# Performance work log

Measured on AMD Instinct MI355X. Metric: run time of the kernel, lower is better.

Reference implementation:

```python
import jax, jax.numpy as jnp
import numpy as np

DIM_MODEL = 1024
NUM_HEADS = 16
DROPOUT_P = 0.5
SCALE = float(np.sqrt(DIM_MODEL // NUM_HEADS))  # NOTE: source MULTIPLIES by this (unusual but faithful)
DROP_KEY = jax.random.key(42)


def setup_inputs() -> dict:
    key = jax.random.key(0)
    ks = jax.random.split(key, 9)
    B, LQ, LK, D = 4, 2048, 2048, DIM_MODEL
    s = 1.0 / np.sqrt(D)
    return {
        "query": jax.random.normal(ks[0], (B, LQ, D), jnp.float32),
        "key": jax.random.normal(ks[1], (B, LK, D), jnp.float32),
        "value": jax.random.normal(ks[2], (B, LK, D), jnp.float32),
        "Wq": jax.random.normal(ks[3], (D, D), jnp.float32) * s,
        "bq": jax.random.normal(ks[4], (D,), jnp.float32) * s,
        "Wk": jax.random.normal(ks[5], (D, D), jnp.float32) * s,
        "bk": jax.random.normal(ks[6], (D,), jnp.float32) * s,
        "Wv": jax.random.normal(ks[7], (D, D), jnp.float32) * s,
        "bv": jax.random.normal(ks[8], (D,), jnp.float32) * s,
    }


def reference(query, key, value, Wq, bq, Wk, bk, Wv, bv):
    # Linear projections (W stored as [in, out])
    q = jnp.einsum('bqd,de->bqe', query, Wq) + bq
    k = jnp.einsum('bkd,de->bke', key, Wk) + bk
    v = jnp.einsum('bkd,de->bke', value, Wv) + bv
    # scores scaled by MULTIPLYING sqrt(d_head), per source
    scores = jnp.einsum('bqe,bke->bqk', q, k) * SCALE
    probs = jax.nn.softmax(scores, axis=-1)
    # dropout (train mode, p=0.5), deterministic fixed key for reproducibility
    keep = jax.random.bernoulli(DROP_KEY, 1.0 - DROPOUT_P, probs.shape)
    probs = jnp.where(keep, probs / (1.0 - DROPOUT_P), 0.0)
    return jnp.einsum('bqk,bke->bqe', probs, v)
```

## Files before the change

### kernel.cpp

```cpp
#include <hip/hip_runtime.h>
#include <math.h>

#define BATCH  4
#define LSEQ   2048
#define DMODEL 1024
#define MROWS  (BATCH * LSEQ)
#define SCORE_SCALE 8.0f

#define THREEFRY_PARTITIONABLE 1

typedef __bf16 bf16_t;
typedef bf16_t bf16x8 __attribute__((ext_vector_type(8)));
typedef bf16_t bf16x4 __attribute__((ext_vector_type(4)));
typedef float  f32x4  __attribute__((ext_vector_type(4)));

#define LDSP(p) ((__attribute__((address_space(3))) void*)(p))
#define GLBP(p) ((const __attribute__((address_space(1))) void*)(p))

__device__ __forceinline__ unsigned rotl32(unsigned x, int r) {
    return (x << r) | (x >> (32 - r));
}

__device__ __forceinline__ void threefry2x32(unsigned k0, unsigned k1,
                                             unsigned x0, unsigned x1,
                                             unsigned& o0, unsigned& o1) {
    const unsigned ks0 = k0, ks1 = k1, ks2 = k0 ^ k1 ^ 0x1BD11BDAu;
    x0 += ks0; x1 += ks1;
#define TF_R(r) { x0 += x1; x1 = rotl32(x1, r); x1 ^= x0; }
    TF_R(13) TF_R(15) TF_R(26) TF_R(6)
    x0 += ks1; x1 += ks2 + 1u;
    TF_R(17) TF_R(29) TF_R(16) TF_R(24)
    x0 += ks2; x1 += ks0 + 2u;
    TF_R(13) TF_R(15) TF_R(26) TF_R(6)
    x0 += ks0; x1 += ks1 + 3u;
    TF_R(17) TF_R(29) TF_R(16) TF_R(24)
    x0 += ks1; x1 += ks2 + 4u;
    TF_R(13) TF_R(15) TF_R(26) TF_R(6)
    x0 += ks2; x1 += ks0 + 5u;
#undef TF_R
    o0 = x0; o1 = x1;
}

__device__ __forceinline__ bool dropout_keep(unsigned n) {
    unsigned o0, o1;
#if THREEFRY_PARTITIONABLE
    threefry2x32(0u, 42u, 0u, n, o0, o1);
    unsigned bits = o0 ^ o1;
#else
    const unsigned HALF = (unsigned)(BATCH * LSEQ) * (unsigned)LSEQ / 2u;
    unsigned c0 = (n < HALF) ? n : (n - HALF);
    unsigned c1 = (n < HALF) ? (n + HALF) : n;
    threefry2x32(0u, 42u, c0, c1, o0, o1);
    unsigned bits = (n < HALF) ? o0 : o1;
#endif
    return bits < 0x80000000u;
}

__global__ __launch_bounds__(256)
void split_f32(const float* __restrict__ X0, const float* __restrict__ X1,
               bf16_t* __restrict__ hi, bf16_t* __restrict__ lo, int n) {
    const int y = blockIdx.y;
    const float* X = y ? X1 : X0;
    long long i = (long long)(blockIdx.x * 256 + threadIdx.x) * 4;
    if (i >= n) return;
    float4 v = *(const float4*)(X + i);
    bf16x4 h, l;
    h[0] = (bf16_t)v.x; l[0] = (bf16_t)(v.x - (float)h[0]);
    h[1] = (bf16_t)v.y; l[1] = (bf16_t)(v.y - (float)h[1]);
    h[2] = (bf16_t)v.z; l[2] = (bf16_t)(v.z - (float)h[2]);
    h[3] = (bf16_t)v.w; l[3] = (bf16_t)(v.w - (float)h[3]);
    *(bf16x4*)(hi + (long long)y * n + i) = h;
    *(bf16x4*)(lo + (long long)y * n + i) = l;
}

__global__ __launch_bounds__(256)
void cvt_bf16(const float* __restrict__ X, bf16_t* __restrict__ Y, int n) {
    long long i = (long long)(blockIdx.x * 256 + threadIdx.x) * 8;
    if (i >= n) return;
    float4 a = *(const float4*)(X + i);
    float4 b = *(const float4*)(X + i + 4);
    bf16x8 o;
    o[0] = (bf16_t)a.x; o[1] = (bf16_t)a.y; o[2] = (bf16_t)a.z; o[3] = (bf16_t)a.w;
    o[4] = (bf16_t)b.x; o[5] = (bf16_t)b.y; o[6] = (bf16_t)b.z; o[7] = (bf16_t)b.w;
    *(bf16x8*)(Y + i) = o;
}

__global__ __launch_bounds__(256)
void split_transpose(const float* __restrict__ W0, const float* __restrict__ W1,
                     bf16_t* __restrict__ Th, bf16_t* __restrict__ Tl,
                     int Kd, int Nd) {
    __shared__ float t[32][33];
    const int z = blockIdx.z;
    const float* W = z ? W1 : W0;
    const long long zo = (long long)z * Kd * Nd;
    const int bx = blockIdx.x * 32;
    const int by = blockIdx.y * 32;
    const int tx = threadIdx.x & 31, ty = threadIdx.x >> 5;
#pragma unroll
    for (int i = 0; i < 4; ++i)
        t[ty + i * 8][tx] = W[(long long)(by + ty + i * 8) * Nd + bx + tx];
    __syncthreads();
#pragma unroll
    for (int i = 0; i < 4; ++i) {
        float v = t[tx][ty + i * 8];
        long long idx = zo + (long long)(bx + ty + i * 8) * Kd + by + tx;
        bf16_t h = (bf16_t)v;
        Th[idx] = h;
        Tl[idx] = (bf16_t)(v - (float)h);
    }
}

template <int SPLIT, int OUT, int BROW>
__global__ __launch_bounds__(256)
void gemm_mfma(const bf16_t* __restrict__ Ah, const bf16_t* __restrict__ Al,
               const bf16_t* __restrict__ Bh, const bf16_t* __restrict__ Bl,
               const float* __restrict__ bias, const float* __restrict__ bias2,
               float* __restrict__ Cf, bf16_t* __restrict__ Ch,
               bf16_t* __restrict__ Cl,
               int M, int N, int K, float scale,
               long long sA, long long sB, long long sC,
               int SX, int NYt) {
    constexpr int TM = 128, TN = 128, TOT = 256, CHUNKS = 4;
    constexpr int NB = SPLIT ? 2 : 1;
    constexpr int BUFSZ = NB * TOT * 32;
    __shared__ __align__(16) bf16_t smem[2 * BUFSZ];

    const int bid = blockIdx.x;
    const int xcd = bid & 7;
    const int ii = bid >> 3;
    const int perz = SX * NYt;
    const int zz = ii / perz;
    const int rr = ii - zz * perz;
    const int nx = xcd + ((rr % SX) << 3);
    const int my = rr / SX;
    const long long z = zz;
    const int m0 = my * TM, n0 = nx * TN;

    const int tid = threadIdx.x;
    const int lane = tid & 63;
    const int wave = tid >> 6;
    const int quad = lane >> 4;
    const int l16 = lane & 15;
    const int wm = (wave & 1) * 64;
    const int wn = (wave >> 1) * 64;

    const bf16_t* gAh = Ah + z * sA;
    const bf16_t* gBh = Bh + z * sB;
    const bf16_t* gAl = SPLIT ? Al + z * sA : nullptr;
    const bf16_t* gBl = SPLIT ? Bl + z * sB : nullptr;

    const int lrow = lane >> 2;
    const int scol = ((lane & 3) ^ ((lrow >> 1) & 3)) * 8;
    const int sw = (l16 >> 1) & 3;

    auto issue = [&](int k0, int b) {
        bf16_t* base = smem + b * BUFSZ;
#pragma unroll
        for (int c = 0; c < CHUNKS; ++c) {
            const int rbase = wave * 64 + c * 16;
            const int row = rbase + lrow;
            if (rbase < TM) {
                const long long g = (long long)(m0 + row) * K + k0 + scol;
                __builtin_amdgcn_global_load_lds(GLBP(gAh + g), LDSP(base + row * 32), 16, 0, 0);
                if constexpr (SPLIT)
                    __builtin_amdgcn_global_load_lds(GLBP(gAl + g), LDSP(base + TOT * 32 + row * 32), 16, 0, 0);
            } else {
                const int br = row - TM;
                const long long g = (long long)(n0 + br) * K + k0 + scol;
                __builtin_amdgcn_global_load_lds(GLBP(gBh + g), LDSP(base + TM * 32 + br * 32), 16, 0, 0);
                if constexpr (SPLIT)
                    __builtin_amdgcn_global_load_lds(GLBP(gBl + g), LDSP(base + TOT * 32 + TM * 32 + br * 32), 16, 0, 0);
            }
        }
    };

    f32x4 acc[4][4];
#pragma unroll
    for (int i = 0; i < 4; ++i)
#pragma unroll
        for (int j = 0; j < 4; ++j)
            acc[i][j] = (f32x4){0.f, 0.f, 0.f, 0.f};

    issue(0, 0);
    const int NIT = K >> 5;
    for (int it = 0; it < NIT; ++it) {
        const int b = it & 1;
        const bool more = (it + 1) < NIT;
        if (more) issue((it + 1) << 5, b ^ 1);
        if constexpr (SPLIT) {
            if (more) asm volatile("s_waitcnt vmcnt(8)" ::: "memory");
            else      asm volatile("s_waitcnt vmcnt(0)" ::: "memory");
        } else {
            if (more) asm volatile("s_waitcnt vmcnt(4)" ::: "memory");
            else      asm volatile("s_waitcnt vmcnt(0)" ::: "memory");
        }
        asm volatile("s_barrier" ::: "memory");

        bf16_t* base = smem + b * BUFSZ;
        bf16_t* sAh = base;
        bf16_t* sBh = base + TM * 32;
        bf16_t* sAl = base + TOT * 32;
        bf16_t* sBl = base + TOT * 32 + TM * 32;

        bf16x8 afh[4], bfh[4], afl[4], bfl[4];
#pragma unroll
        for (int i = 0; i < 4; ++i) {
            const int ao = (wm + i * 16 + l16) * 32 + (quad ^ sw) * 8;
            afh[i] = *(const bf16x8*)(sAh + ao);
            if constexpr (SPLIT) afl[i] = *(const bf16x8*)(sAl + ao);
        }
#pragma unroll
        for (int j = 0; j < 4; ++j) {
            const int bo = (wn + j * 16 + l16) * 32 + (quad ^ sw) * 8;
            bfh[j] = *(const bf16x8*)(sBh + bo);
            if constexpr (SPLIT) bfl[j] = *(const bf16x8*)(sBl + bo);
        }
#pragma unroll
        for (int i = 0; i < 4; ++i)
#pragma unroll
            for (int j = 0; j < 4; ++j) {
                acc[i][j] = __builtin_amdgcn_mfma_f32_16x16x32_bf16(afh[i], bfh[j], acc[i][j], 0, 0, 0);
                if constexpr (SPLIT) {
                    acc[i][j] = __builtin_amdgcn_mfma_f32_16x16x32_bf16(afh[i], bfl[j], acc[i][j], 0, 0, 0);
                    acc[i][j] = __builtin_amdgcn_mfma_f32_16x16x32_bf16(afl[i], bfh[j], acc[i][j], 0, 0, 0);
                }
            }
        asm volatile("s_barrier" ::: "memory");
    }

    const float* bz = (z == 1 && bias2) ? bias2 : bias;
#pragma unroll
    for (int i = 0; i < 4; ++i)
#pragma unroll
        for (int j = 0; j < 4; ++j) {
            const int n = n0 + wn + j * 16 + l16;
            float bvn = 0.f;
            if constexpr (OUT != 0 && !BROW) bvn = bz[n];
#pragma unroll
            for (int r = 0; r < 4; ++r) {
                const int m = m0 + wm + i * 16 + quad * 4 + r;
                const long long idx = z * sC + (long long)m * N + n;
                float v = acc[i][j][r];
                if constexpr (OUT == 0) {
                    Cf[idx] = v * scale;
                } else if constexpr (OUT == 1) {
                    v += bvn;
                    bf16_t h = (bf16_t)v;
                    Ch[idx] = h;
                    Cl[idx] = (bf16_t)(v - (float)h);
                } else {
                    v += BROW ? bz[m] : bvn;
                    Ch[idx] = (bf16_t)v;
                }
            }
        }
}

template <int OUT>
__global__ __launch_bounds__(512, 2)
void gemm_mfma_8ph(const bf16_t* __restrict__ Ah, const bf16_t* __restrict__ Al,
                   const bf16_t* __restrict__ Bh, const bf16_t* __restrict__ Bl,
                   const float* __restrict__ bias, const float* __restrict__ bias2,
                   float* __restrict__ Cf, bf16_t* __restrict__ Ch,
                   bf16_t* __restrict__ Cl,
                   int M, int N, int K, float scale,
                   long long sA, long long sB, long long sC,
                   int NYt, int NZ) {
    constexpr int TM = 256, TN = 256;
    constexpr int PLANE = 256 * 32;
    __shared__ __align__(16) bf16_t smem[2 * 4 * PLANE];

    const int bid = blockIdx.x;
    const int gid = (bid & 7) * 32 + (bid >> 3);
    const int nzy = NZ * NYt;
    const int nx = gid / nzy;
    const int rem = gid - nx * nzy;
    const int zz = rem / NYt;
    const int my = rem - zz * NYt;
    const long long z = zz;
    const int m0 = my * TM, n0 = nx * TN;

    const int tid = threadIdx.x;
    const int lane = tid & 63;
    const int wave = tid >> 6;
    const int quad = lane >> 4;
    const int l16 = lane & 15;
    const int wm = (wave >> 2) * 128;
    const int wn = (wave & 3) * 64;

    const bf16_t* gAh = Ah + z * sA;
    const bf16_t* gAl = Al + z * sA;
    const bf16_t* gBh = Bh + z * sB;
    const bf16_t* gBl = Bl + z * sB;

    const int lrow = lane >> 2;
    const int scol = ((lane & 3) ^ ((lrow >> 1) & 3)) * 8;
    const int sw = (l16 >> 1) & 3;

    auto issue = [&](int k0, int b) {
        bf16_t* base = smem + b * (4 * PLANE);
#pragma unroll
        for (int c = 0; c < 8; ++c) {
            const int s = wave * 8 + c;
            const int p = s >> 4;
            const int row = ((s & 15) << 4) + lrow;
            bf16_t* dst = base + p * PLANE + row * 32;
            const long long ka = (long long)(m0 + row) * K + k0 + scol;
            const long long kb = (long long)(n0 + row) * K + k0 + scol;
            if (p == 0)
                __builtin_amdgcn_global_load_lds(GLBP(gAh + ka), LDSP(dst), 16, 0, 0);
            else if (p == 1)
                __builtin_amdgcn_global_load_lds(GLBP(gBh + kb), LDSP(dst), 16, 0, 0);
            else if (p == 2)
                __builtin_amdgcn_global_load_lds(GLBP(gAl + ka), LDSP(dst), 16, 0, 0);
            else
                __builtin_amdgcn_global_load_lds(GLBP(gBl + kb), LDSP(dst), 16, 0, 0);
        }
    };

    f32x4 acc[8][4];
#pragma unroll
    for (int i = 0; i < 8; ++i)
#pragma unroll
        for (int j = 0; j < 4; ++j)
            acc[i][j] = (f32x4){0.f, 0.f, 0.f, 0.f};

    issue(0, 0);
    const int NIT = K >> 5;
    for (int it = 0; it < NIT; ++it) {
        const int b = it & 1;
        const bool more = (it + 1) < NIT;
        if (more) issue((it + 1) << 5, b ^ 1);
        if (more) asm volatile("s_waitcnt vmcnt(8)" ::: "memory");
        else      asm volatile("s_waitcnt vmcnt(0)" ::: "memory");
        asm volatile("s_barrier" ::: "memory");

        bf16_t* base = smem + b * (4 * PLANE);
        bf16_t* sAh = base;
        bf16_t* sBh = base + PLANE;
        bf16_t* sAl = base + 2 * PLANE;
        bf16_t* sBl = base + 3 * PLANE;

        bf16x8 bfh[4], bfl[4];
#pragma unroll
        for (int j = 0; j < 4; ++j) {
            const int bo = (wn + j * 16 + l16) * 32 + (quad ^ sw) * 8;
            bfh[j] = *(const bf16x8*)(sBh + bo);
            bfl[j] = *(const bf16x8*)(sBl + bo);
        }

#pragma unroll
        for (int ph = 0; ph < 4; ++ph) {
            bf16x8 afh[2], afl[2];
#pragma unroll
            for (int i = 0; i < 2; ++i) {
                const int ao = (wm + (ph * 2 + i) * 16 + l16) * 32 + (quad ^ sw) * 8;
                afh[i] = *(const bf16x8*)(sAh + ao);
                afl[i] = *(const bf16x8*)(sAl + ao);
            }
            asm volatile("s_barrier" ::: "memory");
            asm volatile("s_waitcnt lgkmcnt(0)" ::: "memory");
            __builtin_amdgcn_sched_barrier(0);
            __builtin_amdgcn_s_setprio(1);
#pragma unroll
            for (int i = 0; i < 2; ++i)
#pragma unroll
                for (int j = 0; j < 4; ++j) {
                    f32x4 a = acc[ph * 2 + i][j];
                    a = __builtin_amdgcn_mfma_f32_16x16x32_bf16(afh[i], bfh[j], a, 0, 0, 0);
                    a = __builtin_amdgcn_mfma_f32_16x16x32_bf16(afh[i], bfl[j], a, 0, 0, 0);
                    a = __builtin_amdgcn_mfma_f32_16x16x32_bf16(afl[i], bfh[j], a, 0, 0, 0);
                    acc[ph * 2 + i][j] = a;
                }
            __builtin_amdgcn_s_setprio(0);
            asm volatile("s_barrier" ::: "memory");
        }
    }

    const float* bz = (z == 1 && bias2) ? bias2 : bias;
#pragma unroll
    for (int i = 0; i < 8; ++i)
#pragma unroll
        for (int j = 0; j < 4; ++j) {
            const int n = n0 + wn + j * 16 + l16;
            float bvn = 0.f;
            if constexpr (OUT != 0) bvn = bz[n];
#pragma unroll
            for (int r = 0; r < 4; ++r) {
                const int m = m0 + wm + i * 16 + quad * 4 + r;
                const long long idx = z * sC + (long long)m * N + n;
                float v = acc[i][j][r];
                if constexpr (OUT == 0) {
                    Cf[idx] = v * scale;
                } else {
                    v += bvn;
                    bf16_t h = (bf16_t)v;
                    Ch[idx] = h;
                    Cl[idx] = (bf16_t)(v - (float)h);
                }
            }
        }
}

__global__ __launch_bounds__(256)
void softmax_dropout(const float* __restrict__ S, bf16_t* __restrict__ P) {
    const unsigned row = blockIdx.x;
    const float* rp = S + (long long)row * LSEQ;
    const int tid = threadIdx.x;

    float v[8];
    *(float4*)(v)     = *(const float4*)(rp + tid * 8);
    *(float4*)(v + 4) = *(const float4*)(rp + tid * 8 + 4);

    float m = v[0];
#pragma unroll
    for (int e = 1; e < 8; ++e) m = fmaxf(m, v[e]);
#pragma unroll
    for (int o = 1; o < 64; o <<= 1) m = fmaxf(m, __shfl_xor(m, o));
    __shared__ float redm[4];
    if ((tid & 63) == 0) redm[tid >> 6] = m;
    __syncthreads();
    m = fmaxf(fmaxf(redm[0], redm[1]), fmaxf(redm[2], redm[3]));

    float s = 0.f;
#pragma unroll
    for (int e = 0; e < 8; ++e) { v[e] = __expf(v[e] - m); s += v[e]; }
#pragma unroll
    for (int o = 1; o < 64; o <<= 1) s += __shfl_xor(s, o);
    __shared__ float reds[4];
    if ((tid & 63) == 0) reds[tid >> 6] = s;
    __syncthreads();
    s = (reds[0] + reds[1]) + (reds[2] + reds[3]);

    const float inv = 2.0f / s;
    const unsigned nb = row * (unsigned)LSEQ + (unsigned)(tid * 8);
    bf16x8 o8;
#pragma unroll
    for (int e = 0; e < 8; ++e)
        o8[e] = (bf16_t)(dropout_keep(nb + e) ? v[e] * inv : 0.0f);
    *(bf16x8*)(P + (long long)row * LSEQ + tid * 8) = o8;
}

extern "C" void kernel_launch(void* const* d_in, const int* in_sizes, int n_in,
                              void* d_out, int out_size, void* d_ws, size_t ws_size,
                              hipStream_t stream) {
    const float* query = (const float*)d_in[0];
    const float* key_  = (const float*)d_in[1];
    const float* value = (const float*)d_in[2];
    const float* Wq = (const float*)d_in[3];
    const float* bq = (const float*)d_in[4];
    const float* Wk = (const float*)d_in[5];
    const float* bk = (const float*)d_in[6];
    const float* Wv = (const float*)d_in[7];
    const float* bv = (const float*)d_in[8];
    float* out = (float*)d_out;

    char* w = (char*)d_ws;
    const size_t Q1 = (size_t)MROWS * DMODEL * 2;
    bf16_t* Qh  = (bf16_t*)(w);
    bf16_t* Ql  = (bf16_t*)(w + 2 * Q1);
    bf16_t* VT  = (bf16_t*)(w + 4 * Q1);
    float*  S   = (float*)(w + 5 * Q1);
    bf16_t* XvH  = (bf16_t*)(w + 5 * Q1);
    bf16_t* XqkH = (bf16_t*)(w + 5 * Q1);
    bf16_t* XqkL = (bf16_t*)(w + 7 * Q1);
    bf16_t* WTh = (bf16_t*)(w + 9 * Q1);
    bf16_t* WTl = (bf16_t*)(w + 9 * Q1 + 2 * (size_t)DMODEL * DMODEL * 2);
    bf16_t* P   = Qh;

    dim3 b256(256);
    dim3 b512(512);
    const int NELEM = MROWS * DMODEL;
    const long long DD = (long long)DMODEL * DMODEL;
    dim3 gwt1(DMODEL / 32, DMODEL / 32, 1);
    dim3 gwt2(DMODEL / 32, DMODEL / 32, 2);

    split_transpose<<<gwt1, b256, 0, stream>>>(Wv, nullptr, WTh, WTl, DMODEL, DMODEL);
    cvt_bf16<<<dim3(NELEM / 2048), b256, 0, stream>>>(value, XvH, NELEM);
    gemm_mfma<0, 2, 1><<<dim3(512), b256, 0, stream>>>(
        WTh, nullptr, XvH, nullptr, bv, nullptr, nullptr, VT, nullptr,
        DMODEL, LSEQ, DMODEL, 1.f,
        0, (long long)LSEQ * DMODEL, (long long)DMODEL * LSEQ,
        2, DMODEL / 128);

    split_transpose<<<gwt2, b256, 0, stream>>>(Wq, Wk, WTh, WTl, DMODEL, DMODEL);
    split_f32<<<dim3(NELEM / 1024, 2), b256, 0, stream>>>(query, key_, XqkH, XqkL, NELEM);
    gemm_mfma_8ph<1><<<dim3(256), b512, 0, stream>>>(
        XqkH, XqkL, WTh, WTl, bq, bk, nullptr, Qh, Ql,
        MROWS, DMODEL, DMODEL, 1.f,
        (long long)NELEM, DD, (long long)NELEM,
        MROWS / 256, 2);

    gemm_mfma_8ph<0><<<dim3(256), b512, 0, stream>>>(
        Qh, Ql, Qh + NELEM, Ql + NELEM, nullptr, nullptr, S, nullptr, nullptr,
        LSEQ, LSEQ, DMODEL, SCORE_SCALE,
        (long long)LSEQ * DMODEL, (long long)LSEQ * DMODEL,
        (long long)LSEQ * LSEQ,
        LSEQ / 256, 4);

    softmax_dropout<<<dim3(MROWS), b256, 0, stream>>>(S, P);

    gemm_mfma<0, 0, 0><<<dim3(512), b256, 0, stream>>>(
        P, nullptr, VT, nullptr, nullptr, nullptr, out, nullptr, nullptr,
        LSEQ, DMODEL, LSEQ, 1.f,
        (long long)LSEQ * LSEQ, (long long)DMODEL * LSEQ,
        (long long)LSEQ * DMODEL,
        1, LSEQ / 128);
}
```

Baseline: 468.8 us.

## Interleave next-tile global-to-LDS loads across MFMA phases with finer vmcnt waits

Rather than issuing all eight global_load_lds copies for the next K-tile at the top of each iteration, the loads are split into eight rounds, two issued per compute phase, interleaved with the MFMA work. The LDS plane layout is reordered so B planes arrive first and A planes in phase order, with per-phase vmcnt waits that let each phase start once its own slice has landed. The aim is to overlap memory traffic with tensor math and shrink the stall at the start of each iteration. The precise vmcnt counts are fragile: miscounting could introduce races or extra stalls.

```diff
diff --git a/kernel.cpp b/kernel.cpp
--- a/kernel.cpp
+++ b/kernel.cpp
@@ -297,24 +297,21 @@
     const int scol = ((lane & 3) ^ ((lrow >> 1) & 3)) * 8;
     const int sw = (l16 >> 1) & 3;
 
-    auto issue = [&](int k0, int b) {
+    auto stage_round = [&](int r, int k0, int b) {
         bf16_t* base = smem + b * (4 * PLANE);
-#pragma unroll
-        for (int c = 0; c < 8; ++c) {
-            const int s = wave * 8 + c;
-            const int p = s >> 4;
-            const int row = ((s & 15) << 4) + lrow;
-            bf16_t* dst = base + p * PLANE + row * 32;
-            const long long ka = (long long)(m0 + row) * K + k0 + scol;
-            const long long kb = (long long)(n0 + row) * K + k0 + scol;
-            if (p == 0)
-                __builtin_amdgcn_global_load_lds(GLBP(gAh + ka), LDSP(dst), 16, 0, 0);
-            else if (p == 1)
-                __builtin_amdgcn_global_load_lds(GLBP(gBh + kb), LDSP(dst), 16, 0, 0);
-            else if (p == 2)
-                __builtin_amdgcn_global_load_lds(GLBP(gAl + ka), LDSP(dst), 16, 0, 0);
-            else
-                __builtin_amdgcn_global_load_lds(GLBP(gBl + kb), LDSP(dst), 16, 0, 0);
+        if (r < 4) {
+            const int row = ((r & 1) << 7) + (wave << 4) + lrow;
+            const bf16_t* src = (r >= 2) ? gBl : gBh;
+            bf16_t* dst = base + ((r >= 2) ? 3 : 2) * PLANE + row * 32;
+            __builtin_amdgcn_global_load_lds(
+                GLBP(src + (long long)(n0 + row) * K + k0 + scol), LDSP(dst), 16, 0, 0);
+        } else {
+            const int p = r - 4;
+            const int row = (p << 5) + ((wave & 2) ? 128 : 0) + ((wave & 1) << 4) + lrow;
+            const bf16_t* src = (wave >= 4) ? gAl : gAh;
+            bf16_t* dst = base + ((wave >= 4) ? 1 : 0) * PLANE + row * 32;
+            __builtin_amdgcn_global_load_lds(
+                GLBP(src + (long long)(m0 + row) * K + k0 + scol), LDSP(dst), 16, 0, 0);
         }
     };
 
@@ -325,29 +322,23 @@
         for (int j = 0; j < 4; ++j)
             acc[i][j] = (f32x4){0.f, 0.f, 0.f, 0.f};
 
-    issue(0, 0);
+#pragma unroll
+    for (int r = 0; r < 8; ++r) stage_round(r, 0, 0);
+    asm volatile("s_waitcnt vmcnt(3)" ::: "memory");
+    asm volatile("s_barrier" ::: "memory");
+
     const int NIT = K >> 5;
     for (int it = 0; it < NIT; ++it) {
         const int b = it & 1;
         const bool more = (it + 1) < NIT;
-        if (more) issue((it + 1) << 5, b ^ 1);
-        if (more) asm volatile("s_waitcnt vmcnt(8)" ::: "memory");
-        else      asm volatile("s_waitcnt vmcnt(0)" ::: "memory");
-        asm volatile("s_barrier" ::: "memory");
-
+        const int k1 = (it + 1) << 5;
         bf16_t* base = smem + b * (4 * PLANE);
         bf16_t* sAh = base;
-        bf16_t* sBh = base + PLANE;
-        bf16_t* sAl = base + 2 * PLANE;
+        bf16_t* sAl = base + PLANE;
+        bf16_t* sBh = base + 2 * PLANE;
         bf16_t* sBl = base + 3 * PLANE;
 
         bf16x8 bfh[4], bfl[4];
-#pragma unroll
-        for (int j = 0; j < 4; ++j) {
-            const int bo = (wn + j * 16 + l16) * 32 + (quad ^ sw) * 8;
-            bfh[j] = *(const bf16x8*)(sBh + bo);
-            bfl[j] = *(const bf16x8*)(sBl + bo);
-        }
 
 #pragma unroll
         for (int ph = 0; ph < 4; ++ph) {
@@ -358,6 +349,21 @@
                 afh[i] = *(const bf16x8*)(sAh + ao);
                 afl[i] = *(const bf16x8*)(sAl + ao);
             }
+            if (ph == 0) {
+#pragma unroll
+                for (int j = 0; j < 4; ++j) {
+                    const int bo = (wn + j * 16 + l16) * 32 + (quad ^ sw) * 8;
+                    bfh[j] = *(const bf16x8*)(sBh + bo);
+                    bfl[j] = *(const bf16x8*)(sBl + bo);
+                }
+            }
+
+            if (more) {
+                stage_round(ph * 2,     k1, b ^ 1);
+                stage_round(ph * 2 + 1, k1, b ^ 1);
+            }
+
+            if (ph == 0) asm volatile("s_waitcnt lgkmcnt(8)" ::: "memory");
             asm volatile("s_barrier" ::: "memory");
             asm volatile("s_waitcnt lgkmcnt(0)" ::: "memory");
             __builtin_amdgcn_sched_barrier(0);
@@ -373,6 +379,17 @@
                     acc[ph * 2 + i][j] = a;
                 }
             __builtin_amdgcn_s_setprio(0);
+
+            if (more) {
+                if (ph == 0)      asm volatile("s_waitcnt vmcnt(4)" ::: "memory");
+                else if (ph == 1) asm volatile("s_waitcnt vmcnt(5)" ::: "memory");
+                else if (ph == 2) asm volatile("s_waitcnt vmcnt(6)" ::: "memory");
+                else              asm volatile("s_waitcnt vmcnt(3)" ::: "memory");
+            } else {
+                if (ph == 0)      asm volatile("s_waitcnt vmcnt(2)" ::: "memory");
+                else if (ph == 1) asm volatile("s_waitcnt vmcnt(1)" ::: "memory");
+                else if (ph == 2) asm volatile("s_waitcnt vmcnt(0)" ::: "memory");
+            }
             asm volatile("s_barrier" ::: "memory");
         }
     }
```

New measurement: 453.1 us. 1.03x faster.
